# Kernel tuning notes

Measured on AMD Instinct MI355X. Metric: run time of the kernel, lower is better.

## Reference

```python
import jax, jax.numpy as jnp
import numpy as np

B, T, D = 2, 2048, 2048
H, KV, HD = 16, 4, 128          # n_heads, n_kv_heads, head_dim
THETA = 10000.0
NREP = H // KV


def _rope_tables(t, hd, dtype):
    inv_freq = 1.0 / (THETA ** (jnp.arange(0, hd, 2, dtype=jnp.float32) / hd))
    pos = jnp.arange(t, dtype=jnp.float32)
    freqs = jnp.outer(pos, inv_freq)            # [T, hd/2]
    emb = jnp.concatenate([freqs, freqs], -1)   # [T, hd]
    return jnp.cos(emb).astype(dtype), jnp.sin(emb).astype(dtype)


def _rotate_half(x):
    a, b = x[..., : x.shape[-1] // 2], x[..., x.shape[-1] // 2 :]
    return jnp.concatenate([-b, a], axis=-1)


def setup_inputs() -> dict:
    key = jax.random.key(0)
    kx, kq, kk, kv, ko = jax.random.split(key, 5)
    s = 1.0 / np.sqrt(D)
    return {
        "x": jax.random.normal(kx, (B, T, D), jnp.float32),
        "Wq": jax.random.normal(kq, (D, H * HD), jnp.float32) * s,
        "Wk": jax.random.normal(kk, (D, KV * HD), jnp.float32) * s,
        "Wv": jax.random.normal(kv, (D, KV * HD), jnp.float32) * s,
        "Wo": jax.random.normal(ko, (H * HD, D), jnp.float32) * s,
    }


def reference(x, Wq, Wk, Wv, Wo):
    b, t, _ = x.shape
    # QKV projections (bias=False)
    q = (x @ Wq).reshape(b, t, H, HD).transpose(0, 2, 1, 3)    # [B,H,T,hd]
    k = (x @ Wk).reshape(b, t, KV, HD).transpose(0, 2, 1, 3)   # [B,KV,T,hd]
    v = (x @ Wv).reshape(b, t, KV, HD).transpose(0, 2, 1, 3)   # [B,KV,T,hd]

    cos, sin = _rope_tables(t, HD, x.dtype)                    # [T,hd]
    q = q * cos + _rotate_half(q) * sin
    k = k * cos + _rotate_half(k) * sin

    # GQA: group query heads onto shared KV heads (no KV replication)
    qg = q.reshape(b, KV, NREP, t, HD)                         # [B,KV,R,T,hd]
    scale = HD ** -0.5
    scores = jnp.einsum("bgrth,bgsh->bgrts", qg, k) * scale    # [B,KV,R,T,T]
    causal = jnp.tril(jnp.ones((t, t), bool))
    scores = jnp.where(causal, scores, jnp.finfo(scores.dtype).min)
    attn = jax.nn.softmax(scores.astype(jnp.float32), axis=-1).astype(x.dtype)
    out = jnp.einsum("bgrts,bgsh->bgrth", attn, v)             # [B,KV,R,T,hd]
    out = out.reshape(b, H, t, HD).transpose(0, 2, 1, 3).reshape(b, t, H * HD)
    return out @ Wo
```

## Files before the change

### kernel.cpp

```cpp
#include <hip/hip_runtime.h>
#include <hip/hip_bf16.h>

#define B_ 2
#define T_ 2048
#define DM_ 2048
#define H_ 16
#define KV_ 4
#define HD_ 128
#define M_ 4096
#define QKVN 3072

typedef __attribute__((ext_vector_type(8))) short bf16x8;
typedef __attribute__((ext_vector_type(4))) float f32x4;
typedef __attribute__((ext_vector_type(4))) short s16x4;
typedef unsigned short u16;
typedef unsigned int u32;
typedef __attribute__((address_space(1))) unsigned int as1_u32;
typedef __attribute__((address_space(3))) unsigned int as3_u32;

__device__ inline u16 f2b(float f){
  __hip_bfloat16 h = __float2bfloat16(f);
  return *reinterpret_cast<u16*>(&h);
}
__device__ inline float b2f(u16 u){
  __hip_bfloat16 h = *reinterpret_cast<__hip_bfloat16*>(&u);
  return __bfloat162float(h);
}
__device__ inline f32x4 mfma16(bf16x8 a, bf16x8 b, f32x4 c){
  return __builtin_amdgcn_mfma_f32_16x16x32_bf16(a, b, c, 0, 0, 0);
}

__global__ void cvt_f32_bf16(const float* __restrict__ in, u16* __restrict__ out){
  int i = (blockIdx.x*256 + threadIdx.x)*4;
  float4 v = *reinterpret_cast<const float4*>(in + i);
  s16x4 o;
  o[0] = (short)f2b(v.x); o[1] = (short)f2b(v.y);
  o[2] = (short)f2b(v.z); o[3] = (short)f2b(v.w);
  *reinterpret_cast<s16x4*>(out + i) = o;
}

__global__ void transpose_cvt(const float* __restrict__ W, u16* __restrict__ Wt, int K, int N){
  __shared__ float tile[32][33];
  const int n0 = blockIdx.x*32, k0 = blockIdx.y*32;
  const int tx = threadIdx.x, ty = threadIdx.y;
#pragma unroll
  for (int i=0;i<4;i++)
    tile[ty+8*i][tx] = W[(size_t)(k0+ty+8*i)*N + n0 + tx];
  __syncthreads();
#pragma unroll
  for (int i=0;i<4;i++)
    Wt[(size_t)(n0+ty+8*i)*K + k0 + tx] = f2b(tile[tx][ty+8*i]);
}

__global__ void transpose_v(const u16* __restrict__ vb, u16* __restrict__ vt){
  __shared__ u16 tile[32][33];
  const int t0 = blockIdx.x*32, d0 = blockIdx.y*32, bk = blockIdx.z;
  const int bb = bk >> 2, kv = bk & 3;
  const int tx = threadIdx.x, ty = threadIdx.y;
#pragma unroll
  for (int i=0;i<4;i++)
    tile[ty+8*i][tx] = vb[(size_t)(bb*T_ + t0+ty+8*i)*QKVN + kv*HD_ + d0 + tx];
  __syncthreads();
#pragma unroll
  for (int i=0;i<4;i++)
    vt[(size_t)(bk*HD_ + d0+ty+8*i)*T_ + t0 + tx] = tile[tx][ty+8*i];
}

__global__ void rope_table(float2* __restrict__ tab){
  int idx = blockIdx.x*256 + threadIdx.x;
  int t = idx >> 6, d = idx & 63;
  float inv = exp2f((float)d * -0.2076205059304601f);
  float sn, cs;
  sincosf((float)t * inv, &sn, &cs);
  tab[idx] = float2{cs, sn};
}

__global__ void rope_apply(u16* __restrict__ qk, const float2* __restrict__ tab,
                           int lognh, int stride){
  int idx = blockIdx.x*256 + threadIdx.x;
  int dp = idx & 31;
  int rh = idx >> 5;
  int nh = 1 << lognh;
  int h = rh & (nh-1);
  int row = rh >> lognh;
  if (row >= M_) return;
  int t = row & (T_-1);
  float4 cn = *reinterpret_cast<const float4*>(tab + t*64 + 2*dp);
  size_t base = (size_t)row*stride + h*HD_ + 2*dp;
  u32 lo = *reinterpret_cast<const u32*>(qk + base);
  u32 hi = *reinterpret_cast<const u32*>(qk + base + 64);
  float a0 = b2f(lo & 0xffff), a1 = b2f(lo >> 16);
  float b0 = b2f(hi & 0xffff), b1 = b2f(hi >> 16);
  u32 nlo = (u32)f2b(a0*cn.x - b0*cn.y) | ((u32)f2b(a1*cn.z - b1*cn.w) << 16);
  u32 nhi = (u32)f2b(b0*cn.x + a0*cn.y) | ((u32)f2b(b1*cn.z + a1*cn.w) << 16);
  *reinterpret_cast<u32*>(qk + base)      = nlo;
  *reinterpret_cast<u32*>(qk + base + 64) = nhi;
}

__device__ inline void cstore(float* p, float v){ *p = v; }
__device__ inline void cstore(u16* p, float v){ *p = f2b(v); }

template<typename CT>
__global__ __launch_bounds__(256) void gemm_bt(const u16* __restrict__ A, const u16* __restrict__ BT,
                                               CT* __restrict__ C, int M, int N, int K)
{
  __shared__ u16 Als[128*32];
  __shared__ u16 Bls[128*32];
  const int tid = threadIdx.x;
  const int wave = tid>>6, lane = tid&63;
  const int gx = gridDim.x;
  int wid = blockIdx.y*gx + blockIdx.x;
  const int cpx = (gx*gridDim.y) >> 3;
  wid = (wid & 7)*cpx + (wid >> 3);
  const int m0 = (wid / gx)*128, n0 = (wid % gx)*128;
  const int wr = (wave>>1)*64, wc = (wave&1)*64;

  f32x4 acc[4][4];
#pragma unroll
  for (int i=0;i<4;i++)
#pragma unroll
    for (int j=0;j<4;j++) acc[i][j] = f32x4{0.f,0.f,0.f,0.f};

  const int lin0 = ((wave*2+0)*64 + lane)*8;
  const int lin1 = ((wave*2+1)*64 + lane)*8;
  const int r0 = lin0>>5, c0 = lin0&31;
  const int r1 = lin1>>5, c1 = lin1&31;

  for (int k0=0; k0<K; k0+=32){
    __syncthreads();
    __builtin_amdgcn_global_load_lds((as1_u32*)(A  + (size_t)(m0+r0)*K + k0 + c0),
                                     (as3_u32*)(Als + (wave*2+0)*512), 16, 0, 0);
    __builtin_amdgcn_global_load_lds((as1_u32*)(A  + (size_t)(m0+r1)*K + k0 + c1),
                                     (as3_u32*)(Als + (wave*2+1)*512), 16, 0, 0);
    __builtin_amdgcn_global_load_lds((as1_u32*)(BT + (size_t)(n0+r0)*K + k0 + c0),
                                     (as3_u32*)(Bls + (wave*2+0)*512), 16, 0, 0);
    __builtin_amdgcn_global_load_lds((as1_u32*)(BT + (size_t)(n0+r1)*K + k0 + c1),
                                     (as3_u32*)(Bls + (wave*2+1)*512), 16, 0, 0);
    __syncthreads();

    bf16x8 af[4], bfr[4];
#pragma unroll
    for (int mi=0;mi<4;mi++)
      af[mi] = *reinterpret_cast<const bf16x8*>(Als + (wr + mi*16 + (lane&15))*32 + 8*(lane>>4));
#pragma unroll
    for (int ni=0;ni<4;ni++)
      bfr[ni] = *reinterpret_cast<const bf16x8*>(Bls + (wc + ni*16 + (lane&15))*32 + 8*(lane>>4));
#pragma unroll
    for (int mi=0;mi<4;mi++)
#pragma unroll
      for (int ni=0;ni<4;ni++)
        acc[mi][ni] = mfma16(af[mi], bfr[ni], acc[mi][ni]);
  }

#pragma unroll
  for (int mi=0;mi<4;mi++)
#pragma unroll
    for (int ni=0;ni<4;ni++)
#pragma unroll
      for (int j=0;j<4;j++){
        int row = m0 + wr + mi*16 + (lane>>4)*4 + j;
        int col = n0 + wc + ni*16 + (lane&15);
        cstore(C + (size_t)row*N + col, acc[mi][ni][j]);
      }
}

__device__ inline const u16* slot_cptr(const u16* pout, const u16* pwt, int u){
  return (u < 4096) ? (pout + (size_t)u*4096) : (pwt + (size_t)(u-4096)*4096);
}

__global__ __launch_bounds__(256, 2) void attn_kernel(const u16* __restrict__ qkv,
                                                      const u16* __restrict__ Vt,
                                                      u16* __restrict__ pout,
                                                      u16* __restrict__ pwt,
                                                      float* __restrict__ ml,
                                                      u16* __restrict__ ao)
{
  __shared__ u16 Ktile[2][4096];
  __shared__ u16 Vtile[2][4096];
  __shared__ u16 plds[4][32*40];
  const int wave = threadIdx.x>>6, lane = threadIdx.x&63;
  const int g = lane>>4, qc = lane&15;

  const int bh = blockIdx.x & 31;
  const int rem = blockIdx.x >> 5;
  int q4, e;
  if (rem < 4)       { q4=0; e=rem; }
  else if (rem < 12) { q4=1; e=rem-4; }
  else if (rem < 24) { q4=2; e=rem-12; }
  else               { q4=3; e=rem-24; }
  const int j  = q4*4 + e/(q4+1);
  const int c  = e%(q4+1);
  const int nc = q4 + 1;
  const int qt = j*4 + wave;
  const int ntg = j*4 + 4;
  const int tstart = 16*c;
  const int tcnt = min(16, ntg - tstart);

  const int h = bh & (H_-1), b = bh >> 4;
  const int kv = h >> 2;

  const u16* qbase = qkv + (size_t)(b*T_ + qt*32)*QKVN + h*HD_ + 8*g;
  bf16x8 qf[2][4];
#pragma unroll
  for (int qs=0; qs<2; qs++)
#pragma unroll
    for (int d4=0; d4<4; d4++)
      qf[qs][d4] = *reinterpret_cast<const bf16x8*>(qbase + (size_t)(qs*16+qc)*QKVN + d4*32);

  const char* Kbase = (const char*)(qkv + (size_t)(b*T_)*QKVN + 2048 + kv*HD_);
  const char* Vbase = (const char*)(Vt + (size_t)(b*KV_+kv)*HD_*T_);
  const char* Ktc = (const char*)&Ktile[0][0];
  const char* Vtc = (const char*)&Vtile[0][0];

  f32x4 oacc[2][8];
#pragma unroll
  for (int qs=0; qs<2; qs++)
#pragma unroll
    for (int dt=0; dt<8; dt++) oacc[qs][dt] = f32x4{0.f,0.f,0.f,0.f};
  float mrun[2] = {-1e30f, -1e30f};
  float lrun[2] = {0.f, 0.f};
  const float SCALE = 0.08838834764831845f;
  const float L2E = 1.4426950408889634f;
  const float DEFER = 8.f;
  u16* pw = &plds[wave][0];

  auto compute = [&](int t, int half, bool masked){
    const int s0 = t*32;
    const int hb = half*8192;
    f32x4 sacc[2][2];
#pragma unroll
    for (int qs=0; qs<2; qs++)
#pragma unroll
      for (int ss=0; ss<2; ss++) sacc[qs][ss] = f32x4{0.f,0.f,0.f,0.f};
    __builtin_amdgcn_s_setprio(1);
#pragma unroll
    for (int d4=0; d4<4; d4++)
#pragma unroll
      for (int ss=0; ss<2; ss++){
        int A = ((ss*16+qc)<<8) + (d4<<6) + (g<<4);
        A ^= (qc&7)<<4;
        bf16x8 kf = *reinterpret_cast<const bf16x8*>(Ktc + hb + A);
#pragma unroll
        for (int qs=0; qs<2; qs++)
          sacc[qs][ss] = mfma16(kf, qf[qs][d4], sacc[qs][ss]);
      }
    __builtin_amdgcn_s_setprio(0);

    float p[2][8], al[2], mnew[2];
#pragma unroll
    for (int qs=0; qs<2; qs++){
      float tm = -1e30f;
#pragma unroll
      for (int ss=0; ss<2; ss++)
#pragma unroll
        for (int jj=0; jj<4; jj++){
          float v = sacc[qs][ss][jj]*SCALE;
          if (masked){
            int sg = s0 + ss*16 + g*4 + jj;
            if (sg > qt*32 + qs*16 + qc) v = -1e30f;
          }
          p[qs][ss*4+jj] = v;
          tm = fmaxf(tm, v);
        }
      tm = fmaxf(tm, __shfl_xor(tm, 16));
      tm = fmaxf(tm, __shfl_xor(tm, 32));
      mnew[qs] = fmaxf(mrun[qs], tm);
      if (tm - mrun[qs] <= DEFER) mnew[qs] = mrun[qs];
      al[qs] = exp2f((mrun[qs]-mnew[qs])*L2E);
    }
#pragma unroll
    for (int qs=0; qs<2; qs++){
      float rs = 0.f;
#pragma unroll
      for (int i=0;i<8;i++){ p[qs][i] = exp2f((p[qs][i]-mnew[qs])*L2E); rs += p[qs][i]; }
      rs += __shfl_xor(rs, 16);
      rs += __shfl_xor(rs, 32);
      lrun[qs] = lrun[qs]*al[qs] + rs;
      mrun[qs] = mnew[qs];
    }
    if (!__all((al[0]==1.f) & (al[1]==1.f))){
      float aj0[4], aj1[4];
#pragma unroll
      for (int jj=0; jj<4; jj++){
        aj0[jj] = __shfl(al[0], g*4+jj);
        aj1[jj] = __shfl(al[1], g*4+jj);
      }
#pragma unroll
      for (int dt=0; dt<8; dt++)
#pragma unroll
        for (int jj=0; jj<4; jj++){
          oacc[0][dt][jj] *= aj0[jj];
          oacc[1][dt][jj] *= aj1[jj];
        }
    }
#pragma unroll
    for (int qs=0; qs<2; qs++)
#pragma unroll
      for (int ss=0; ss<2; ss++){
        unsigned w0 = (unsigned)f2b(p[qs][ss*4+0]) | ((unsigned)f2b(p[qs][ss*4+1])<<16);
        unsigned w1 = (unsigned)f2b(p[qs][ss*4+2]) | ((unsigned)f2b(p[qs][ss*4+3])<<16);
        *reinterpret_cast<unsigned*>(pw + (qs*16+qc)*40 + ss*16 + g*4)     = w0;
        *reinterpret_cast<unsigned*>(pw + (qs*16+qc)*40 + ss*16 + g*4 + 2) = w1;
      }
    bf16x8 pf[2];
#pragma unroll
    for (int qs=0; qs<2; qs++)
      pf[qs] = *reinterpret_cast<const bf16x8*>(pw + (qs*16+qc)*40 + 8*g);
    __builtin_amdgcn_s_setprio(1);
#pragma unroll
    for (int dt=0; dt<8; dt++){
      int A = ((dt*16+qc)<<6) + (g<<4);
      A ^= ((qc>>1)&3)<<4;
      bf16x8 vf = *reinterpret_cast<const bf16x8*>(Vtc + hb + A);
#pragma unroll
      for (int qs=0; qs<2; qs++)
        oacc[qs][dt] = mfma16(pf[qs], vf, oacc[qs][dt]);
    }
    __builtin_amdgcn_s_setprio(0);
  };

  const int npair = (tcnt+1)>>1;
  for (int ip = 0; ip < npair; ip++){
    const int t0 = tstart + 2*ip;
    const int ntile = min(2, tstart + tcnt - t0);
    __syncthreads();
#pragma unroll
    for (int tt=0; tt<2; tt++){
      if (tt < ntile){
        const size_t r0 = (size_t)(t0+tt)*32;
#pragma unroll
        for (int c2=0; c2<2; c2++){
          const int cc = wave*2 + c2;
          const int D = cc*1024 + lane*16;
          {
            const int LK = D ^ (((D>>8)&7)<<4);
            const char* src = Kbase + (r0 + (size_t)(D>>8))*(QKVN*2) + (LK & 255);
            __builtin_amdgcn_global_load_lds((as1_u32*)src,
              (as3_u32*)((char*)&Ktile[0][0] + tt*8192 + cc*1024), 16, 0, 0);
          }
          {
            const int LV = (D&63) ^ (((D>>7)&3)<<4);
            const char* src = Vbase + ((size_t)(D>>6)*T_ + r0 + (LV>>1))*2;
            __builtin_amdgcn_global_load_lds((as1_u32*)src,
              (as3_u32*)((char*)&Vtile[0][0] + tt*8192 + cc*1024), 16, 0, 0);
          }
        }
      }
    }
    __syncthreads();
    if (t0 <= qt)                 compute(t0,   0, t0   == qt);
    if (ntile > 1 && t0+1 <= qt)  compute(t0+1, 1, t0+1 == qt);
  }

  if (nc == 1){
    float lj0[4], lj1[4];
    float li0 = 1.f/lrun[0], li1 = 1.f/lrun[1];
#pragma unroll
    for (int jj=0; jj<4; jj++){
      lj0[jj] = __shfl(li0, g*4+jj);
      lj1[jj] = __shfl(li1, g*4+jj);
    }
    u16* ob = ao + (size_t)(b*T_ + qt*32)*(H_*HD_) + h*HD_;
#pragma unroll
    for (int dt=0; dt<8; dt++)
#pragma unroll
      for (int jj=0; jj<4; jj++){
        ob[(size_t)(g*4+jj)*(H_*HD_) + dt*16 + qc]      = f2b(oacc[0][dt][jj]*lj0[jj]);
        ob[(size_t)(16 + g*4+jj)*(H_*HD_) + dt*16 + qc] = f2b(oacc[1][dt][jj]*lj1[jj]);
      }
  } else {
    int off;
    if (qt < 32)      off = (qt-16)*2;
    else if (qt < 48) off = 32 + (qt-32)*3;
    else              off = 80 + (qt-48)*4;
    const int u = bh*144 + off + c;
    u16* ob = (u < 4096) ? (pout + (size_t)u*4096) : (pwt + (size_t)(u-4096)*4096);
#pragma unroll
    for (int qs=0; qs<2; qs++)
#pragma unroll
      for (int dt=0; dt<8; dt++)
#pragma unroll
        for (int jj=0; jj<4; jj++)
          ob[(size_t)(qs*16 + g*4+jj)*128 + dt*16 + qc] = f2b(oacc[qs][dt][jj]);
    if (lane < 16){
      float* mlb = ml + (size_t)u*64;
#pragma unroll
      for (int qs=0; qs<2; qs++){
        mlb[qs*16 + lane]      = mrun[qs];
        mlb[32 + qs*16 + lane] = lrun[qs];
      }
    }
  }
}

__global__ void combine_kernel(const u16* __restrict__ pout, const u16* __restrict__ pwt,
                               const float* __restrict__ ml, u16* __restrict__ ao)
{
  const float L2E = 1.4426950408889634f;
  int idx = blockIdx.x*256 + threadIdx.x;
  int dg = idx & 15;
  int r  = (idx >> 4) & 31;
  int t  = idx >> 9;
  int bh = t/48, qi = t%48;
  int qt = 16 + qi;
  int nc, off;
  if (qt < 32)      { nc = 2; off = (qt-16)*2; }
  else if (qt < 48) { nc = 3; off = 32 + (qt-32)*3; }
  else              { nc = 4; off = 80 + (qt-48)*4; }
  const int ubase = bh*144 + off;

  float m[4], l[4];
  float M = -1e30f;
#pragma unroll 4
  for (int cc=0; cc<4; cc++){
    if (cc < nc){
      m[cc] = ml[(size_t)(ubase+cc)*64 + r];
      l[cc] = ml[(size_t)(ubase+cc)*64 + 32 + r];
      M = fmaxf(M, m[cc]);
    }
  }
  float acc[8];
#pragma unroll
  for (int i=0;i<8;i++) acc[i] = 0.f;
  float denom = 0.f;
#pragma unroll 4
  for (int cc=0; cc<4; cc++){
    if (cc < nc){
      float w = exp2f((m[cc]-M)*L2E);
      denom += w*l[cc];
      const u16* sp = slot_cptr(pout, pwt, ubase+cc);
      bf16x8 v8 = *reinterpret_cast<const bf16x8*>(sp + (size_t)r*128 + dg*8);
#pragma unroll
      for (int i=0;i<8;i++) acc[i] += w*b2f((u16)v8[i]);
    }
  }
  float inv = 1.f/denom;
  bf16x8 o;
#pragma unroll
  for (int i=0;i<8;i++) o[i] = (short)f2b(acc[i]*inv);
  int b = bh >> 4, h = bh & 15;
  size_t row = (size_t)b*T_ + qt*32 + r;
  *reinterpret_cast<bf16x8*>(ao + row*2048 + h*128 + dg*8) = o;
}

extern "C" void kernel_launch(void* const* d_in, const int* in_sizes, int n_in,
                              void* d_out, int out_size, void* d_ws, size_t ws_size,
                              hipStream_t stream)
{
  const float* x  = (const float*)d_in[0];
  const float* Wq = (const float*)d_in[1];
  const float* Wk = (const float*)d_in[2];
  const float* Wv = (const float*)d_in[3];
  const float* Wo = (const float*)d_in[4];
  float* out = (float*)d_out;

  char* ws = (char*)d_ws;
  size_t off = 0;
  auto carve = [&](size_t bytes)->void*{
    void* p = ws + off; off += (bytes + 255) & ~(size_t)255; return p;
  };
  u16*    xb   = (u16*)carve((size_t)M_*DM_*2);
  u16*    wT   = (u16*)carve((size_t)QKVN*2048*2);
  u16*    woT  = (u16*)carve((size_t)2048*2048*2);
  u16*    qkv  = (u16*)carve((size_t)M_*QKVN*2);
  u16*    vt   = (u16*)carve((size_t)M_*512*2);
  float2* tab  = (float2*)carve((size_t)T_*64*8);
  float*  ml   = (float*)carve((size_t)4608*64*4);
  u16*    ao   = xb;
  u16*    pout = (u16*)d_out;
  u16*    pwt  = wT;

  cvt_f32_bf16<<<8192, 256, 0, stream>>>(x, xb);
  rope_table<<<512, 256, 0, stream>>>(tab);
  transpose_cvt<<<dim3(64,64), dim3(32,8), 0, stream>>>(Wq, wT,               2048, 2048);
  transpose_cvt<<<dim3(16,64), dim3(32,8), 0, stream>>>(Wk, wT + 2048*2048,   2048, 512);
  transpose_cvt<<<dim3(16,64), dim3(32,8), 0, stream>>>(Wv, wT + 2560*2048,   2048, 512);
  transpose_cvt<<<dim3(64,64), dim3(32,8), 0, stream>>>(Wo, woT,              2048, 2048);

  gemm_bt<u16><<<dim3(24,32), 256, 0, stream>>>(xb, wT, qkv, M_, QKVN, 2048);

  rope_apply<<<8192, 256, 0, stream>>>(qkv,        tab, 4, QKVN);
  rope_apply<<<2048, 256, 0, stream>>>(qkv + 2048, tab, 2, QKVN);

  transpose_v<<<dim3(64,4,8), dim3(32,8), 0, stream>>>(qkv + 2560, vt);

  attn_kernel<<<1280, 256, 0, stream>>>(qkv, vt, pout, pwt, ml, ao);
  combine_kernel<<<3072, 256, 0, stream>>>(pout, pwt, ml, ao);

  gemm_bt<float><<<dim3(16,32), 256, 0, stream>>>(ao, woT, out, M_, 2048, 2048);
}
```

Measured before the change: 262.0 us.

## Deepen GEMM K-tile to 64 with XOR-swizzled LDS layout

Doubles the K depth of each LDS tile in the bf16 GEMM from 32 to 64, halving the number of barrier pairs and load rounds per output tile. It also XOR-swizzles the 16-byte column chunks by row so that the fragment reads, now on a 128-byte row stride, avoid LDS bank conflicts. LDS use per block doubles to 32 KB, which may lower occupancy, and more fragment registers are held per iteration.

```diff
diff --git a/kernel.cpp b/kernel.cpp
--- a/kernel.cpp
+++ b/kernel.cpp
@@ -104,10 +104,11 @@
 __global__ __launch_bounds__(256) void gemm_bt(const u16* __restrict__ A, const u16* __restrict__ BT,
                                                CT* __restrict__ C, int M, int N, int K)
 {
-  __shared__ u16 Als[128*32];
-  __shared__ u16 Bls[128*32];
+  __shared__ u16 Als[128*64];
+  __shared__ u16 Bls[128*64];
   const int tid = threadIdx.x;
   const int wave = tid>>6, lane = tid&63;
+  const int gl = lane>>4, qcl = lane&15;
   const int gx = gridDim.x;
   int wid = blockIdx.y*gx + blockIdx.x;
   const int cpx = (gx*gridDim.y) >> 3;
@@ -121,35 +122,47 @@
 #pragma unroll
     for (int j=0;j<4;j++) acc[i][j] = f32x4{0.f,0.f,0.f,0.f};
 
-  const int lin0 = ((wave*2+0)*64 + lane)*8;
-  const int lin1 = ((wave*2+1)*64 + lane)*8;
-  const int r0 = lin0>>5, c0 = lin0&31;
-  const int r1 = lin1>>5, c1 = lin1&31;
-
-  for (int k0=0; k0<K; k0+=32){
+  int rowD[4], colD[4];
+#pragma unroll
+  for (int p=0;p<4;p++){
+    const int D = p*4096 + tid*16;
+    rowD[p] = D>>7;
+    colD[p] = ((((D>>4)&7) ^ (rowD[p]&7)))*8;
+  }
+
+  for (int k0=0; k0<K; k0+=64){
     __syncthreads();
-    __builtin_amdgcn_global_load_lds((as1_u32*)(A  + (size_t)(m0+r0)*K + k0 + c0),
-                                     (as3_u32*)(Als + (wave*2+0)*512), 16, 0, 0);
-    __builtin_amdgcn_global_load_lds((as1_u32*)(A  + (size_t)(m0+r1)*K + k0 + c1),
-                                     (as3_u32*)(Als + (wave*2+1)*512), 16, 0, 0);
-    __builtin_amdgcn_global_load_lds((as1_u32*)(BT + (size_t)(n0+r0)*K + k0 + c0),
-                                     (as3_u32*)(Bls + (wave*2+0)*512), 16, 0, 0);
-    __builtin_amdgcn_global_load_lds((as1_u32*)(BT + (size_t)(n0+r1)*K + k0 + c1),
-                                     (as3_u32*)(Bls + (wave*2+1)*512), 16, 0, 0);
+#pragma unroll
+    for (int p=0;p<4;p++){
+      __builtin_amdgcn_global_load_lds((as1_u32*)(A  + (size_t)(m0+rowD[p])*K + k0 + colD[p]),
+                                       (as3_u32*)((char*)Als + p*4096 + wave*1024), 16, 0, 0);
+      __builtin_amdgcn_global_load_lds((as1_u32*)(BT + (size_t)(n0+rowD[p])*K + k0 + colD[p]),
+                                       (as3_u32*)((char*)Bls + p*4096 + wave*1024), 16, 0, 0);
+    }
     __syncthreads();
 
-    bf16x8 af[4], bfr[4];
+    bf16x8 af[4][2], bfr[4][2];
 #pragma unroll
     for (int mi=0;mi<4;mi++)
-      af[mi] = *reinterpret_cast<const bf16x8*>(Als + (wr + mi*16 + (lane&15))*32 + 8*(lane>>4));
+#pragma unroll
+      for (int kk=0;kk<2;kk++){
+        const int row = wr + mi*16 + qcl;
+        af[mi][kk] = *reinterpret_cast<const bf16x8*>((char*)Als + row*128 + (((kk<<2)+gl) ^ (qcl&7))*16);
+      }
 #pragma unroll
     for (int ni=0;ni<4;ni++)
-      bfr[ni] = *reinterpret_cast<const bf16x8*>(Bls + (wc + ni*16 + (lane&15))*32 + 8*(lane>>4));
+#pragma unroll
+      for (int kk=0;kk<2;kk++){
+        const int row = wc + ni*16 + qcl;
+        bfr[ni][kk] = *reinterpret_cast<const bf16x8*>((char*)Bls + row*128 + (((kk<<2)+gl) ^ (qcl&7))*16);
+      }
 #pragma unroll
     for (int mi=0;mi<4;mi++)
 #pragma unroll
       for (int ni=0;ni<4;ni++)
-        acc[mi][ni] = mfma16(af[mi], bfr[ni], acc[mi][ni]);
+#pragma unroll
+        for (int kk=0;kk<2;kk++)
+          acc[mi][ni] = mfma16(af[mi][kk], bfr[ni][kk], acc[mi][ni]);
   }
 
 #pragma unroll
```

Result: faster. 249.7 us (-4.7%).
